# Optimization experiments

Hardware: AMD Instinct MI355X
Metric: run time of the kernel (lower is better)

## Reference

```python
import jax, jax.numpy as jnp
import numpy as np

B, S, HID, NH = 2, 2048, 2048, 16
DH = HID // NH  # 128


def _rope_tables(seq_len, dim, dtype=jnp.float32):
    inv_freq = 1.0 / (10000.0 ** (jnp.arange(0, dim, 2, dtype=jnp.float32) / dim))
    t = jnp.arange(seq_len, dtype=jnp.float32)
    freqs = jnp.einsum('i,j->ij', t, inv_freq)          # [S, dim/2]
    emb = jnp.concatenate([freqs, freqs], axis=-1)       # [S, dim]
    return jnp.cos(emb)[None, None].astype(dtype), jnp.sin(emb)[None, None].astype(dtype)


def _rotate_half(x):
    x1, x2 = x[..., : x.shape[-1] // 2], x[..., x.shape[-1] // 2 :]
    return jnp.concatenate([-x2, x1], axis=-1)


def setup_inputs() -> dict:
    key = jax.random.key(0)
    ks = jax.random.split(key, 6)
    hidden_states = jax.random.normal(ks[0], (B, S, HID), dtype=jnp.float32)
    scale = 1.0 / np.sqrt(HID)
    Wq = jax.random.normal(ks[1], (HID, HID), dtype=jnp.float32) * scale
    Wk = jax.random.normal(ks[2], (HID, HID), dtype=jnp.float32) * scale
    Wv = jax.random.normal(ks[3], (HID, HID), dtype=jnp.float32) * scale
    Wo = jax.random.normal(ks[4], (HID, HID), dtype=jnp.float32) * scale
    bq = jnp.zeros((HID,), jnp.float32)
    bk = jnp.zeros((HID,), jnp.float32)
    bv = jnp.zeros((HID,), jnp.float32)
    bo = jnp.zeros((HID,), jnp.float32)
    # causal additive mask [1,1,S,S]
    causal = jnp.tril(jnp.ones((S, S), dtype=bool))
    attention_mask = jnp.where(causal, 0.0, -1e9).astype(jnp.float32)[None, None]
    return dict(hidden_states=hidden_states, attention_mask=attention_mask,
                Wq=Wq, bq=bq, Wk=Wk, bk=bk, Wv=Wv, bv=bv, Wo=Wo, bo=bo)


def reference(hidden_states, attention_mask, Wq, bq, Wk, bk, Wv, bv, Wo, bo):
    b, s, _ = hidden_states.shape
    # torch Linear: x @ W.T + b
    q = (hidden_states @ Wq.T + bq).reshape(b, s, NH, DH).transpose(0, 2, 1, 3)
    k = (hidden_states @ Wk.T + bk).reshape(b, s, NH, DH).transpose(0, 2, 1, 3)
    v = (hidden_states @ Wv.T + bv).reshape(b, s, NH, DH).transpose(0, 2, 1, 3)
    cos, sin = _rope_tables(s, DH)
    q = q * cos + _rotate_half(q) * sin
    k = k * cos + _rotate_half(k) * sin
    scores = jnp.einsum('bhqd,bhkd->bhqk', q * (DH ** -0.5), k)
    scores = scores + attention_mask
    probs = jax.nn.softmax(scores, axis=-1)  # dropout: eval mode (identity)
    out = jnp.einsum('bhqk,bhkd->bhqd', probs, v)
    out = out.transpose(0, 2, 1, 3).reshape(b, s, HID)
    return out @ Wo.T + bo
```

## Files before the change

### kernel.cpp

```cpp
#include <hip/hip_runtime.h>
#include <hip/hip_bf16.h>
#include <cstdint>
#include <cstddef>

#define BB 2
#define SS 2048
#define HH 2048
#define NHH 16
#define DHH 128

using f32x4  = __attribute__((ext_vector_type(4))) float;
using bf16x8 = __attribute__((ext_vector_type(8))) __bf16;
using bf16x4 = __attribute__((ext_vector_type(4))) __bf16;
using bfloat = __bf16;

__device__ inline void gload_lds16(const void* g, void* l) {
    __builtin_amdgcn_global_load_lds(
        (const __attribute__((address_space(1))) void*)g,
        (__attribute__((address_space(3))) void*)l, 16, 0, 0);
}

__device__ inline f32x4 mfma16(bf16x8 a, bf16x8 b, f32x4 c) {
    return __builtin_amdgcn_mfma_f32_16x16x32_bf16(a, b, c, 0, 0, 0);
}

template <int CTRL>
__device__ inline float dpp_max_step(float x) {
    int y = __builtin_amdgcn_update_dpp(0, __builtin_bit_cast(int, x), CTRL, 0xf, 0xf, false);
    return fmaxf(x, __builtin_bit_cast(float, y));
}
__device__ inline float rowmax16(float x) {
    x = dpp_max_step<0x121>(x);
    x = dpp_max_step<0x122>(x);
    x = dpp_max_step<0x124>(x);
    x = dpp_max_step<0x128>(x);
    return x;
}

__global__ void cvt_bf16(const float* __restrict__ in, bfloat* __restrict__ out, int n4) {
    int i = blockIdx.x * blockDim.x + threadIdx.x;
    if (i >= n4) return;
    float4 v = reinterpret_cast<const float4*>(in)[i];
    bf16x4 o;
    o[0] = (bfloat)v.x; o[1] = (bfloat)v.y; o[2] = (bfloat)v.z; o[3] = (bfloat)v.w;
    reinterpret_cast<bf16x4*>(out)[i] = o;
}

__global__ void cvt_bf16_w(const float* __restrict__ s0, const float* __restrict__ s1,
                           const float* __restrict__ s2, const float* __restrict__ s3,
                           bfloat* __restrict__ d0, bfloat* __restrict__ d1,
                           bfloat* __restrict__ d2, bfloat* __restrict__ d3) {
    int sel = blockIdx.x >> 12;
    int i = (blockIdx.x & 4095) * 256 + threadIdx.x;
    const float* s = sel == 0 ? s0 : sel == 1 ? s1 : sel == 2 ? s2 : s3;
    bfloat* d = sel == 0 ? d0 : sel == 1 ? d1 : sel == 2 ? d2 : d3;
    float4 v = reinterpret_cast<const float4*>(s)[i];
    bf16x4 o;
    o[0] = (bfloat)v.x; o[1] = (bfloat)v.y; o[2] = (bfloat)v.z; o[3] = (bfloat)v.w;
    reinterpret_cast<bf16x4*>(d)[i] = o;
}

__global__ void rope_table(float* __restrict__ cosT, float* __restrict__ sinT) {
    int i = blockIdx.x * blockDim.x + threadIdx.x;
    if (i >= SS * 64) return;
    int s = i >> 6, j = i & 63;
    float invf = powf(10000.0f, -(float)j / 64.0f);
    float ang = (float)s * invf;
    cosT[i] = cosf(ang);
    sinT[i] = sinf(ang);
}

__device__ __forceinline__ void kloop256(const bfloat* __restrict__ Ag,
                                         const bfloat* __restrict__ Bg,
                                         f32x4 (&acc)[4][4]) {
    constexpr int K = HH, NT = K / 64;
    __shared__ bfloat Abuf[3][256 * 64];
    __shared__ bfloat Bbuf[3][128 * 64];
    const int t = threadIdx.x, l = t & 63, lr = l & 15, lg = l >> 4;
    const int wid = t >> 6, wr = wid >> 1, wc = wid & 1;
    const int dstu = (t & ~63);

    auto stage = [&](int buf, int kt) {
#pragma unroll
        for (int i = 0; i < 4; i++) {
            int U = i * 512 + t, row = U >> 3, u = (U & 7) ^ (row & 7);
            gload_lds16(Ag + (size_t)row * K + kt * 64 + u * 8,
                        &Abuf[buf][(i * 512 + dstu) * 8]);
        }
#pragma unroll
        for (int i = 0; i < 2; i++) {
            int U = i * 512 + t, row = U >> 3, u = (U & 7) ^ (row & 7);
            gload_lds16(Bg + (size_t)row * K + kt * 64 + u * 8,
                        &Bbuf[buf][(i * 512 + dstu) * 8]);
        }
    };

    int cmap[4];
#pragma unroll
    for (int n = 0; n < 4; n++)
        cmap[n] = (n < 2) ? wc * 32 + n * 16 : 64 + wc * 32 + (n - 2) * 16;
    const int usw0 = lg ^ (lr & 7);
    const int usw1 = (4 + lg) ^ (lr & 7);

    stage(0, 0);
    stage(1, 1);

#pragma unroll 1
    for (int kt = 0; kt < NT; ++kt) {
        const int buf = kt % 3;
        if (kt + 2 < NT) {
            stage((kt + 2) % 3, kt + 2);
            asm volatile("s_waitcnt vmcnt(12)" ::: "memory");
        } else if (kt + 1 < NT) {
            asm volatile("s_waitcnt vmcnt(6)" ::: "memory");
        } else {
            asm volatile("s_waitcnt vmcnt(0)" ::: "memory");
        }
        __builtin_amdgcn_s_barrier();
        __builtin_amdgcn_sched_barrier(0);

        const bfloat* Ab = Abuf[buf];
        const bfloat* Bb = Bbuf[buf];
        bf16x8 af[4][2], bfr[4][2];
#pragma unroll
        for (int m = 0; m < 4; m++) {
            int row = wr * 64 + m * 16 + lr;
            af[m][0] = *reinterpret_cast<const bf16x8*>(&Ab[row * 64 + usw0 * 8]);
            af[m][1] = *reinterpret_cast<const bf16x8*>(&Ab[row * 64 + usw1 * 8]);
        }
#pragma unroll
        for (int n = 0; n < 4; n++) {
            int row = cmap[n] + lr;
            bfr[n][0] = *reinterpret_cast<const bf16x8*>(&Bb[row * 64 + usw0 * 8]);
            bfr[n][1] = *reinterpret_cast<const bf16x8*>(&Bb[row * 64 + usw1 * 8]);
        }
        __builtin_amdgcn_s_setprio(1);
#pragma unroll
        for (int m = 0; m < 4; m++)
#pragma unroll
            for (int n = 0; n < 4; n++) {
                acc[m][n] = mfma16(af[m][0], bfr[n][0], acc[m][n]);
                acc[m][n] = mfma16(af[m][1], bfr[n][1], acc[m][n]);
            }
        __builtin_amdgcn_s_setprio(0);
        __builtin_amdgcn_sched_barrier(0);
        __builtin_amdgcn_s_barrier();
    }
}

__global__ __launch_bounds__(512, 2)
void gemm_qkv(const bfloat* __restrict__ A,
              const bfloat* __restrict__ Bq, const bfloat* __restrict__ Bk,
              const bfloat* __restrict__ Bv,
              const float* __restrict__ bq, const float* __restrict__ bk,
              const float* __restrict__ bv,
              bfloat* __restrict__ Qo, bfloat* __restrict__ Ko, bfloat* __restrict__ Vto,
              const float* __restrict__ cosT, const float* __restrict__ sinT) {
    constexpr int K = HH, N = HH;
    const int sel = blockIdx.y >> 4;
    const bfloat* Bt = sel == 0 ? Bq : sel == 1 ? Bk : Bv;
    const float* bias = sel == 0 ? bq : sel == 1 ? bk : bv;
    const int m0 = blockIdx.x * 256, n0 = (blockIdx.y & 15) * 128;

    f32x4 acc[4][4] = {};
    kloop256(A + (size_t)m0 * K, Bt + (size_t)n0 * K, acc);

    const int t = threadIdx.x, l = t & 63, lr = l & 15, lg = l >> 4;
    const int wid = t >> 6, wr = wid >> 1, wc = wid & 1;

    if (sel == 2) {
#pragma unroll
        for (int m = 0; m < 4; m++) {
            int row = m0 + wr * 64 + m * 16 + lg * 4;
#pragma unroll
            for (int n = 0; n < 4; n++) {
                int cm = (n < 2) ? wc * 32 + n * 16 : 64 + wc * 32 + (n - 2) * 16;
                int col = n0 + cm + lr;
                float bv_ = bias[col];
#pragma unroll
                for (int j = 0; j < 4; j++) {
                    int r = row + j;
                    Vto[((size_t)((r >> 11) * HH + col)) * SS + (r & (SS - 1))] =
                        (bfloat)(acc[m][n][j] + bv_);
                }
            }
        }
    } else {
        bfloat* C = sel == 0 ? Qo : Ko;
        const float qs = sel == 0 ? 0.088388347648318447f : 1.0f;
#pragma unroll
        for (int m = 0; m < 4; m++) {
            int row = m0 + wr * 64 + m * 16 + lg * 4;
#pragma unroll
            for (int n = 0; n < 2; n++) {
                int d = wc * 32 + n * 16 + lr;
                int col1 = n0 + d, col2 = col1 + 64;
                float b1 = bias[col1], b2 = bias[col2];
#pragma unroll
                for (int j = 0; j < 4; j++) {
                    int r = row + j, s = r & (SS - 1);
                    float c  = cosT[s * 64 + d];
                    float sn = sinT[s * 64 + d];
                    float x1 = acc[m][n][j] + b1;
                    float x2 = acc[m][n + 2][j] + b2;
                    C[(size_t)r * N + col1] = (bfloat)((x1 * c - x2 * sn) * qs);
                    C[(size_t)r * N + col2] = (bfloat)((x2 * c + x1 * sn) * qs);
                }
            }
        }
    }
}

__global__ __launch_bounds__(512, 2)
void gemm_out(const bfloat* __restrict__ A, const bfloat* __restrict__ Bt,
              const float* __restrict__ bias, float* __restrict__ C) {
    constexpr int K = HH, N = HH;
    const int m0 = blockIdx.x * 256, n0 = blockIdx.y * 128;

    f32x4 acc[4][4] = {};
    kloop256(A + (size_t)m0 * K, Bt + (size_t)n0 * K, acc);

    const int t = threadIdx.x, l = t & 63, lr = l & 15, lg = l >> 4;
    const int wid = t >> 6, wr = wid >> 1, wc = wid & 1;
#pragma unroll
    for (int m = 0; m < 4; m++) {
        int row = m0 + wr * 64 + m * 16 + lg * 4;
#pragma unroll
        for (int n = 0; n < 4; n++) {
            int cm = (n < 2) ? wc * 32 + n * 16 : 64 + wc * 32 + (n - 2) * 16;
            int col = n0 + cm + lr;
            float bv = bias[col];
#pragma unroll
            for (int j = 0; j < 4; j++)
                C[(size_t)(row + j) * N + col] = acc[m][n][j] + bv;
        }
    }
}

__global__ __launch_bounds__(256, 4)
void attn_fwd(const bfloat* __restrict__ Q, const bfloat* __restrict__ K,
              const bfloat* __restrict__ Vt, bfloat* __restrict__ O) {
    __shared__ bfloat Ks[64 * 128];
    __shared__ bfloat Vs[128 * 64];
    __shared__ bfloat Pw[4][16 * 64];

    const int t = threadIdx.x, w = t >> 6, l = t & 63;
    const int lr = l & 15, lg = l >> 4;
    const int swz = (lr & 7) << 4;

    const int f = blockIdx.x;
    const int xcd = f & 7, slot = f >> 3;
    const int bh = xcd + 8 * (slot >> 5);
    const int qidx = 31 - (slot & 31);
    const int b = bh >> 4, h = bh & 15;
    const int q0 = qidx * 64 + w * 16;

    const size_t bo_ = (size_t)b * SS * HH + (size_t)h * DHH;
    const bfloat* Qp = Q + bo_;
    const bfloat* Kp = K + bo_;
    const bfloat* Vp = Vt + (size_t)(b * NHH + h) * DHH * SS;
    bfloat* Op = O + bo_;

    auto stage = [&](int kv0) {
#pragma unroll
        for (int i = 0; i < 4; i++) {
            int Ub = (i * 4 + w) * 64;
            int U = Ub + l;
            int r = U >> 4;
            int u = (U & 15) ^ (r & 7);
            gload_lds16(Kp + (size_t)(kv0 + r) * HH + u * 8, &Ks[Ub * 8]);
        }
#pragma unroll
        for (int i = 0; i < 4; i++) {
            int Ub = (i * 4 + w) * 64;
            int U = Ub + l;
            int r = U >> 3;
            int u = (U & 7) ^ (r & 7);
            gload_lds16(Vp + (size_t)r * SS + kv0 + u * 8, &Vs[Ub * 8]);
        }
    };

    bf16x8 qf[4];
#pragma unroll
    for (int kt = 0; kt < 4; kt++)
        qf[kt] = *reinterpret_cast<const bf16x8*>(Qp + (size_t)(q0 + lr) * HH + kt * 32 + lg * 8);

    bf16x8 ones;
#pragma unroll
    for (int e = 0; e < 8; e++) ones[e] = (bfloat)1.0f;

    f32x4 o[8] = {};
    f32x4 lsv = {};
    float m[4];
#pragma unroll
    for (int j = 0; j < 4; j++) m[j] = -1e30f;

    const int nkv = qidx + 1;

    for (int kv = 0; kv < nkv; ++kv) {
        stage(kv * 64);
        __syncthreads();

        const char* KB = (const char*)&Ks[0];
        const char* VB = (const char*)&Vs[0];

        f32x4 sc[4] = {};
        __builtin_amdgcn_s_setprio(1);
#pragma unroll
        for (int kt = 0; kt < 4; kt++) {
            const int col = (kt * 64 + lg * 16);
#pragma unroll
            for (int kb = 0; kb < 4; kb++) {
                bf16x8 kf = *reinterpret_cast<const bf16x8*>(
                    KB + (kb * 16 + lr) * 256 + (col ^ swz));
                sc[kb] = mfma16(qf[kt], kf, sc[kb]);
            }
        }
        __builtin_amdgcn_s_setprio(0);

        const bool diag = (kv == nkv - 1);
        float p[4][4], alpha[4];
        bool ga = false;
#pragma unroll
        for (int j = 0; j < 4; j++) {
            float v0 = sc[0][j], v1 = sc[1][j], v2 = sc[2][j], v3 = sc[3][j];
            if (diag) {
                int qr = q0 + lg * 4 + j;
                int k0 = kv * 64 + lr;
                if (k0      > qr) v0 = -1e30f;
                if (k0 + 16 > qr) v1 = -1e30f;
                if (k0 + 32 > qr) v2 = -1e30f;
                if (k0 + 48 > qr) v3 = -1e30f;
            }
            float mx = rowmax16(fmaxf(fmaxf(v0, v1), fmaxf(v2, v3)));
            bool grow = mx > m[j] + 8.0f;
            float mn = grow ? mx : m[j];
            alpha[j] = grow ? __expf(m[j] - mn) : 1.0f;
            m[j] = mn;
            ga = ga || grow;
            p[0][j] = __expf(v0 - mn);
            p[1][j] = __expf(v1 - mn);
            p[2][j] = __expf(v2 - mn);
            p[3][j] = __expf(v3 - mn);
        }
        if (__any(ga)) {
#pragma unroll
            for (int j = 0; j < 4; j++) {
                lsv[j] *= alpha[j];
#pragma unroll
                for (int nt = 0; nt < 8; nt++) o[nt][j] *= alpha[j];
            }
        }

        char* pwb = (char*)&Pw[w][0];
#pragma unroll
        for (int j = 0; j < 4; j++) {
            int q = lg * 4 + j;
            int qs = (q & 7) << 4;
#pragma unroll
            for (int kb = 0; kb < 4; kb++)
                *(bfloat*)(pwb + q * 128 + ((kb * 32 + lr * 2) ^ qs)) = (bfloat)p[kb][j];
        }
        asm volatile("s_waitcnt lgkmcnt(0)" ::: "memory");
        __builtin_amdgcn_sched_barrier(0);

        const char* pwr = (const char*)&Pw[w][0];
        bf16x8 pa0 = *reinterpret_cast<const bf16x8*>(pwr + lr * 128 + ((lg * 16) ^ swz));
        bf16x8 pa1 = *reinterpret_cast<const bf16x8*>(pwr + lr * 128 + ((64 + lg * 16) ^ swz));
        __builtin_amdgcn_s_setprio(1);
        lsv = mfma16(pa0, ones, lsv);
        lsv = mfma16(pa1, ones, lsv);
#pragma unroll
        for (int nt = 0; nt < 8; nt++) {
            const char* vb = VB + (nt * 16 + lr) * 128;
            bf16x8 vf0 = *reinterpret_cast<const bf16x8*>(vb + ((lg * 16) ^ swz));
            bf16x8 vf1 = *reinterpret_cast<const bf16x8*>(vb + ((64 + lg * 16) ^ swz));
            o[nt] = mfma16(pa0, vf0, o[nt]);
            o[nt] = mfma16(pa1, vf1, o[nt]);
        }
        __builtin_amdgcn_s_setprio(0);
        __syncthreads();
    }

#pragma unroll
    for (int j = 0; j < 4; j++) {
        float inv = 1.0f / lsv[j];
        int row = q0 + lg * 4 + j;
#pragma unroll
        for (int nt = 0; nt < 8; nt++)
            Op[(size_t)row * HH + nt * 16 + lr] = (bfloat)(o[nt][j] * inv);
    }
}

extern "C" void kernel_launch(void* const* d_in, const int* in_sizes, int n_in,
                              void* d_out, int out_size, void* d_ws, size_t ws_size,
                              hipStream_t stream) {
    (void)in_sizes; (void)n_in; (void)out_size; (void)ws_size;
    const float* hs = (const float*)d_in[0];
    const float* Wq = (const float*)d_in[2];
    const float* bq = (const float*)d_in[3];
    const float* Wk = (const float*)d_in[4];
    const float* bk = (const float*)d_in[5];
    const float* Wv = (const float*)d_in[6];
    const float* bv = (const float*)d_in[7];
    const float* Wo = (const float*)d_in[8];
    const float* bo = (const float*)d_in[9];

    char* ws = (char*)d_ws;
    size_t off = 0;
    auto alloc = [&](size_t bytes) { void* p = ws + off; off += (bytes + 255) & ~(size_t)255; return p; };
    const size_t MK = (size_t)BB * SS * HH;
    const size_t NK = (size_t)HH * HH;

    bfloat* Xb  = (bfloat*)alloc(MK * 2);
    bfloat* Wqb = (bfloat*)alloc(NK * 2);
    bfloat* Wkb = (bfloat*)alloc(NK * 2);
    bfloat* Wvb = (bfloat*)alloc(NK * 2);
    bfloat* Wob = (bfloat*)alloc(NK * 2);
    bfloat* Qb  = (bfloat*)alloc(MK * 2);
    bfloat* Kb  = (bfloat*)alloc(MK * 2);
    bfloat* Vtb = (bfloat*)alloc(MK * 2);
    float*  cosT = (float*)alloc((size_t)SS * 64 * 4);
    float*  sinT = (float*)alloc((size_t)SS * 64 * 4);
    bfloat* AOb = Xb;

    cvt_bf16<<<(int)(MK / 4 / 256), 256, 0, stream>>>(hs, Xb, (int)(MK / 4));
    cvt_bf16_w<<<4 * 4096, 256, 0, stream>>>(Wq, Wk, Wv, Wo, Wqb, Wkb, Wvb, Wob);
    rope_table<<<(SS * 64 + 255) / 256, 256, 0, stream>>>(cosT, sinT);

    gemm_qkv<<<dim3(BB * SS / 256, 48), 512, 0, stream>>>(
        Xb, Wqb, Wkb, Wvb, bq, bk, bv, Qb, Kb, Vtb, cosT, sinT);

    attn_fwd<<<1024, 256, 0, stream>>>(Qb, Kb, Vtb, AOb);

    gemm_out<<<dim3(BB * SS / 256, HH / 128), 512, 0, stream>>>(
        AOb, Wob, bo, (float*)d_out);
}
```

Baseline: 311.1 us.

## Switch GEMMs to 256x256 tiles with double buffering and 2x4 warp layout

The QKV and output projection GEMMs now use 256x256 block tiles instead of 256x128. Each warp computes a 128x64 sub-tile with 8x4 MFMA accumulators, and the A fragments are loaded in two halves to limit register pressure. LDS staging drops from triple to double buffering so the larger B tile fits in shared memory. This raises arithmetic intensity per loaded byte, at the cost of fewer blocks (16x24 and 16x8 grids), higher register use that may break the 2-blocks/SM launch bound, and less latency hiding.

```diff
diff --git a/kernel.cpp b/kernel.cpp
--- a/kernel.cpp
+++ b/kernel.cpp
@@ -70,80 +70,88 @@
     sinT[i] = sinf(ang);
 }
 
-__device__ __forceinline__ void kloop256(const bfloat* __restrict__ Ag,
-                                         const bfloat* __restrict__ Bg,
-                                         f32x4 (&acc)[4][4]) {
+__device__ __forceinline__ int cmap256(int wc, int nf) {
+    return (wc >> 1) * 128 + (wc & 1) * 32 + (nf & 1) * 16 + (nf >> 1) * 64;
+}
+
+__device__ __forceinline__ void kloop256sq(const bfloat* __restrict__ Ag,
+                                           const bfloat* __restrict__ Bg,
+                                           f32x4 (&acc)[8][4]) {
     constexpr int K = HH, NT = K / 64;
-    __shared__ bfloat Abuf[3][256 * 64];
-    __shared__ bfloat Bbuf[3][128 * 64];
+    __shared__ bfloat Ab[2][256 * 64];
+    __shared__ bfloat Bb[2][256 * 64];
     const int t = threadIdx.x, l = t & 63, lr = l & 15, lg = l >> 4;
-    const int wid = t >> 6, wr = wid >> 1, wc = wid & 1;
-    const int dstu = (t & ~63);
+    const int wid = t >> 6, wr = wid >> 2, wc = wid & 3;
+    const int dstu = t & ~63;
 
     auto stage = [&](int buf, int kt) {
 #pragma unroll
         for (int i = 0; i < 4; i++) {
             int U = i * 512 + t, row = U >> 3, u = (U & 7) ^ (row & 7);
             gload_lds16(Ag + (size_t)row * K + kt * 64 + u * 8,
-                        &Abuf[buf][(i * 512 + dstu) * 8]);
-        }
-#pragma unroll
-        for (int i = 0; i < 2; i++) {
+                        &Ab[buf][(i * 512 + dstu) * 8]);
+        }
+#pragma unroll
+        for (int i = 0; i < 4; i++) {
             int U = i * 512 + t, row = U >> 3, u = (U & 7) ^ (row & 7);
             gload_lds16(Bg + (size_t)row * K + kt * 64 + u * 8,
-                        &Bbuf[buf][(i * 512 + dstu) * 8]);
+                        &Bb[buf][(i * 512 + dstu) * 8]);
         }
     };
 
-    int cmap[4];
-#pragma unroll
-    for (int n = 0; n < 4; n++)
-        cmap[n] = (n < 2) ? wc * 32 + n * 16 : 64 + wc * 32 + (n - 2) * 16;
-    const int usw0 = lg ^ (lr & 7);
-    const int usw1 = (4 + lg) ^ (lr & 7);
+    int brow[4];
+#pragma unroll
+    for (int nf = 0; nf < 4; nf++) brow[nf] = cmap256(wc, nf) + lr;
+    const int usw[2] = { lg ^ (lr & 7), (4 + lg) ^ (lr & 7) };
 
     stage(0, 0);
-    stage(1, 1);
 
 #pragma unroll 1
     for (int kt = 0; kt < NT; ++kt) {
-        const int buf = kt % 3;
-        if (kt + 2 < NT) {
-            stage((kt + 2) % 3, kt + 2);
-            asm volatile("s_waitcnt vmcnt(12)" ::: "memory");
-        } else if (kt + 1 < NT) {
-            asm volatile("s_waitcnt vmcnt(6)" ::: "memory");
+        const int buf = kt & 1;
+        if (kt + 1 < NT) {
+            stage(buf ^ 1, kt + 1);
+            asm volatile("s_waitcnt vmcnt(8)" ::: "memory");
         } else {
             asm volatile("s_waitcnt vmcnt(0)" ::: "memory");
         }
         __builtin_amdgcn_s_barrier();
         __builtin_amdgcn_sched_barrier(0);
 
-        const bfloat* Ab = Abuf[buf];
-        const bfloat* Bb = Bbuf[buf];
-        bf16x8 af[4][2], bfr[4][2];
-#pragma unroll
-        for (int m = 0; m < 4; m++) {
-            int row = wr * 64 + m * 16 + lr;
-            af[m][0] = *reinterpret_cast<const bf16x8*>(&Ab[row * 64 + usw0 * 8]);
-            af[m][1] = *reinterpret_cast<const bf16x8*>(&Ab[row * 64 + usw1 * 8]);
-        }
-#pragma unroll
-        for (int n = 0; n < 4; n++) {
-            int row = cmap[n] + lr;
-            bfr[n][0] = *reinterpret_cast<const bf16x8*>(&Bb[row * 64 + usw0 * 8]);
-            bfr[n][1] = *reinterpret_cast<const bf16x8*>(&Bb[row * 64 + usw1 * 8]);
-        }
-        __builtin_amdgcn_s_setprio(1);
-#pragma unroll
-        for (int m = 0; m < 4; m++)
-#pragma unroll
-            for (int n = 0; n < 4; n++) {
-                acc[m][n] = mfma16(af[m][0], bfr[n][0], acc[m][n]);
-                acc[m][n] = mfma16(af[m][1], bfr[n][1], acc[m][n]);
-            }
-        __builtin_amdgcn_s_setprio(0);
-        __builtin_amdgcn_sched_barrier(0);
+        const bfloat* A_ = Ab[buf];
+        const bfloat* B_ = Bb[buf];
+#pragma unroll
+        for (int ks = 0; ks < 2; ++ks) {
+            bf16x8 bfrag[4];
+#pragma unroll
+            for (int nf = 0; nf < 4; nf++)
+                bfrag[nf] = *reinterpret_cast<const bf16x8*>(&B_[brow[nf] * 64 + usw[ks] * 8]);
+            bf16x8 afr[4];
+#pragma unroll
+            for (int mf = 0; mf < 4; mf++)
+                afr[mf] = *reinterpret_cast<const bf16x8*>(
+                    &A_[(wr * 128 + mf * 16 + lr) * 64 + usw[ks] * 8]);
+            __builtin_amdgcn_s_setprio(1);
+#pragma unroll
+            for (int mf = 0; mf < 4; mf++)
+#pragma unroll
+                for (int nf = 0; nf < 4; nf++)
+                    acc[mf][nf] = mfma16(afr[mf], bfrag[nf], acc[mf][nf]);
+            __builtin_amdgcn_s_setprio(0);
+            __builtin_amdgcn_sched_barrier(0);
+#pragma unroll
+            for (int mf = 0; mf < 4; mf++)
+                afr[mf] = *reinterpret_cast<const bf16x8*>(
+                    &A_[(wr * 128 + (mf + 4) * 16 + lr) * 64 + usw[ks] * 8]);
+            __builtin_amdgcn_s_setprio(1);
+#pragma unroll
+            for (int mf = 0; mf < 4; mf++)
+#pragma unroll
+                for (int nf = 0; nf < 4; nf++)
+                    acc[mf + 4][nf] = mfma16(afr[mf], bfrag[nf], acc[mf + 4][nf]);
+            __builtin_amdgcn_s_setprio(0);
+            __builtin_amdgcn_sched_barrier(0);
+        }
         __builtin_amdgcn_s_barrier();
     }
 }
@@ -157,52 +165,52 @@
               bfloat* __restrict__ Qo, bfloat* __restrict__ Ko, bfloat* __restrict__ Vto,
               const float* __restrict__ cosT, const float* __restrict__ sinT) {
     constexpr int K = HH, N = HH;
-    const int sel = blockIdx.y >> 4;
+    const int sel = blockIdx.y >> 3;
     const bfloat* Bt = sel == 0 ? Bq : sel == 1 ? Bk : Bv;
     const float* bias = sel == 0 ? bq : sel == 1 ? bk : bv;
-    const int m0 = blockIdx.x * 256, n0 = (blockIdx.y & 15) * 128;
-
-    f32x4 acc[4][4] = {};
-    kloop256(A + (size_t)m0 * K, Bt + (size_t)n0 * K, acc);
+    const int m0 = blockIdx.x * 256, n0 = (blockIdx.y & 7) * 256;
+
+    f32x4 acc[8][4] = {};
+    kloop256sq(A + (size_t)m0 * K, Bt + (size_t)n0 * K, acc);
 
     const int t = threadIdx.x, l = t & 63, lr = l & 15, lg = l >> 4;
-    const int wid = t >> 6, wr = wid >> 1, wc = wid & 1;
+    const int wid = t >> 6, wr = wid >> 2, wc = wid & 3;
 
     if (sel == 2) {
 #pragma unroll
-        for (int m = 0; m < 4; m++) {
-            int row = m0 + wr * 64 + m * 16 + lg * 4;
-#pragma unroll
-            for (int n = 0; n < 4; n++) {
-                int cm = (n < 2) ? wc * 32 + n * 16 : 64 + wc * 32 + (n - 2) * 16;
-                int col = n0 + cm + lr;
+        for (int mf = 0; mf < 8; mf++) {
+            int row = m0 + wr * 128 + mf * 16 + lg * 4;
+#pragma unroll
+            for (int nf = 0; nf < 4; nf++) {
+                int col = n0 + cmap256(wc, nf) + lr;
                 float bv_ = bias[col];
 #pragma unroll
                 for (int j = 0; j < 4; j++) {
                     int r = row + j;
                     Vto[((size_t)((r >> 11) * HH + col)) * SS + (r & (SS - 1))] =
-                        (bfloat)(acc[m][n][j] + bv_);
+                        (bfloat)(acc[mf][nf][j] + bv_);
                 }
             }
         }
     } else {
         bfloat* C = sel == 0 ? Qo : Ko;
         const float qs = sel == 0 ? 0.088388347648318447f : 1.0f;
-#pragma unroll
-        for (int m = 0; m < 4; m++) {
-            int row = m0 + wr * 64 + m * 16 + lg * 4;
-#pragma unroll
-            for (int n = 0; n < 2; n++) {
-                int d = wc * 32 + n * 16 + lr;
-                int col1 = n0 + d, col2 = col1 + 64;
+        const int hbase = n0 + (wc >> 1) * 128;
+#pragma unroll
+        for (int mf = 0; mf < 8; mf++) {
+            int row = m0 + wr * 128 + mf * 16 + lg * 4;
+#pragma unroll
+            for (int nf = 0; nf < 2; nf++) {
+                int d = (wc & 1) * 32 + nf * 16 + lr;
+                int col1 = hbase + d, col2 = col1 + 64;
                 float b1 = bias[col1], b2 = bias[col2];
 #pragma unroll
                 for (int j = 0; j < 4; j++) {
                     int r = row + j, s = r & (SS - 1);
                     float c  = cosT[s * 64 + d];
                     float sn = sinT[s * 64 + d];
-                    float x1 = acc[m][n][j] + b1;
-                    float x2 = acc[m][n + 2][j] + b2;
+                    float x1 = acc[mf][nf][j] + b1;
+                    float x2 = acc[mf][nf + 2][j] + b2;
                     C[(size_t)r * N + col1] = (bfloat)((x1 * c - x2 * sn) * qs);
                     C[(size_t)r * N + col2] = (bfloat)((x2 * c + x1 * sn) * qs);
                 }
@@ -215,24 +223,23 @@
 void gemm_out(const bfloat* __restrict__ A, const bfloat* __restrict__ Bt,
               const float* __restrict__ bias, float* __restrict__ C) {
     constexpr int K = HH, N = HH;
-    const int m0 = blockIdx.x * 256, n0 = blockIdx.y * 128;
-
-    f32x4 acc[4][4] = {};
-    kloop256(A + (size_t)m0 * K, Bt + (size_t)n0 * K, acc);
+    const int m0 = blockIdx.x * 256, n0 = blockIdx.y * 256;
+
+    f32x4 acc[8][4] = {};
+    kloop256sq(A + (size_t)m0 * K, Bt + (size_t)n0 * K, acc);
 
     const int t = threadIdx.x, l = t & 63, lr = l & 15, lg = l >> 4;
-    const int wid = t >> 6, wr = wid >> 1, wc = wid & 1;
-#pragma unroll
-    for (int m = 0; m < 4; m++) {
-        int row = m0 + wr * 64 + m * 16 + lg * 4;
-#pragma unroll
-        for (int n = 0; n < 4; n++) {
-            int cm = (n < 2) ? wc * 32 + n * 16 : 64 + wc * 32 + (n - 2) * 16;
-            int col = n0 + cm + lr;
+    const int wid = t >> 6, wr = wid >> 2, wc = wid & 3;
+#pragma unroll
+    for (int mf = 0; mf < 8; mf++) {
+        int row = m0 + wr * 128 + mf * 16 + lg * 4;
+#pragma unroll
+        for (int nf = 0; nf < 4; nf++) {
+            int col = n0 + cmap256(wc, nf) + lr;
             float bv = bias[col];
 #pragma unroll
             for (int j = 0; j < 4; j++)
-                C[(size_t)(row + j) * N + col] = acc[m][n][j] + bv;
+                C[(size_t)(row + j) * N + col] = acc[mf][nf][j] + bv;
         }
     }
 }
@@ -428,11 +435,11 @@
     cvt_bf16_w<<<4 * 4096, 256, 0, stream>>>(Wq, Wk, Wv, Wo, Wqb, Wkb, Wvb, Wob);
     rope_table<<<(SS * 64 + 255) / 256, 256, 0, stream>>>(cosT, sinT);
 
-    gemm_qkv<<<dim3(BB * SS / 256, 48), 512, 0, stream>>>(
+    gemm_qkv<<<dim3(BB * SS / 256, 24), 512, 0, stream>>>(
         Xb, Wqb, Wkb, Wvb, bq, bk, bv, Qb, Kb, Vtb, cosT, sinT);
 
     attn_fwd<<<1024, 256, 0, stream>>>(Qb, Kb, Vtb, AOb);
 
-    gemm_out<<<dim3(BB * SS / 256, HH / 128), 512, 0, stream>>>(
+    gemm_out<<<dim3(BB * SS / 256, HH / 256), 512, 0, stream>>>(
         AOb, Wob, bo, (float*)d_out);
 }
```

Result: slower. 329.5 us (+5.9%).
